# Kernel tuning notes

Measured on AMD Instinct MI355X. Metric: run time of the kernel, lower is better.

The kernel has to match this reference:

```python
import jax, jax.numpy as jnp
import numpy as np

B, L, C = 4, 6400, 768
HS, WS = 80, 80
NH, NP, NL = 6, 4, 1
DH = C // NH
EPS = 1e-6


def setup_inputs() -> dict:
    key = jax.random.key(0)
    ks = jax.random.split(key, 10)
    p = lambda k, shape: jax.random.normal(k, shape, jnp.float32) * 0.02
    return {
        "x": jax.random.normal(ks[0], (B, L, C), jnp.float32),
        "reference_points": jax.random.uniform(ks[1], (B, L, NL, 2), dtype=jnp.float32),
        "feat": jax.random.normal(ks[2], (B, L, C), jnp.float32),
        "spatial_shapes": jnp.array([[HS, WS]], jnp.int32),
        "level_start_index": jnp.array([0], jnp.int32),
        "qn_w": jnp.ones((C,), jnp.float32), "qn_b": jnp.zeros((C,), jnp.float32),
        "fn_w": jnp.ones((C,), jnp.float32), "fn_b": jnp.zeros((C,), jnp.float32),
        "gamma": p(ks[3], (C,)),
        "Wv": p(ks[4], (C, C)), "bv": jnp.zeros((C,), jnp.float32),
        "Woff": p(ks[5], (C, NH * NL * NP * 2)), "boff": p(ks[6], (NH * NL * NP * 2,)),
        "Waw": p(ks[7], (C, NH * NL * NP)), "baw": jnp.zeros((NH * NL * NP,), jnp.float32),
        "Wout": p(ks[8], (C, C)), "bout": jnp.zeros((C,), jnp.float32),
    }


def layernorm(x, w, b):
    mu = jnp.mean(x, -1, keepdims=True)
    var = jnp.mean((x - mu) ** 2, -1, keepdims=True)
    return (x - mu) * jax.lax.rsqrt(var + EPS) * w + b


def ms_deform_attn(q, reference_points, f, spatial_shapes, level_start_index,
                   Wv, bv, Woff, boff, Waw, baw, Wout, bout):
    shapes = np.asarray(spatial_shapes)      # static metadata (concrete)
    starts = np.asarray(level_start_index)
    value = (f @ Wv + bv).reshape(B, L, NH, DH)
    offs = (q @ Woff + boff).reshape(B, L, NH, NL, NP, 2)
    aw = jax.nn.softmax((q @ Waw + baw).reshape(B, L, NH, NL * NP), axis=-1)
    aw = aw.reshape(B, L, NH, NL, NP)
    # offset normalizer is (W, H) per level
    normalizer = jnp.stack([spatial_shapes[:, 1], spatial_shapes[:, 0]], -1).astype(q.dtype)
    loc = reference_points[:, :, None, :, None, :] + offs / normalizer[None, None, None, :, None, :]

    gat = jax.vmap(jax.vmap(lambda vv, ii: vv[ii]))  # over batch, then head
    levels = []
    for l in range(shapes.shape[0]):
        H_, W_ = int(shapes[l, 0]), int(shapes[l, 1])
        s0 = int(starts[l])
        v = value[:, s0:s0 + H_ * W_].transpose(0, 2, 1, 3)  # [B,NH,HW,DH]
        # grid_sample align_corners=False pixel coords
        lx = loc[:, :, :, l, :, 0] * W_ - 0.5                # [B,L,NH,NP]
        ly = loc[:, :, :, l, :, 1] * H_ - 0.5
        x0 = jnp.floor(lx); y0 = jnp.floor(ly)
        tx, ty = lx - x0, ly - y0
        x0i, y0i = x0.astype(jnp.int32), y0.astype(jnp.int32)
        acc = jnp.zeros((B, NH, L, NP, DH), value.dtype)
        for dy, wy in ((0, 1.0 - ty), (1, ty)):
            for dx, wx in ((0, 1.0 - tx), (1, tx)):
                xi, yi = x0i + dx, y0i + dy
                valid = (xi >= 0) & (xi < W_) & (yi >= 0) & (yi < H_)  # zero padding
                idx = (jnp.clip(yi, 0, H_ - 1) * W_ + jnp.clip(xi, 0, W_ - 1)).transpose(0, 2, 1, 3)
                w = (wx * wy * valid).transpose(0, 2, 1, 3)           # [B,NH,L,NP]
                acc = acc + gat(v, idx) * w[..., None]
        levels.append(acc)                                            # [B,NH,L,NP,DH]
    samp = jnp.stack(levels, axis=3)                                  # [B,NH,L,NL,NP,DH]
    out = jnp.einsum('bhqlpd,bqhlp->bqhd', samp, aw).reshape(B, L, C)
    return out @ Wout + bout


def reference(x, reference_points, feat, spatial_shapes, level_start_index,
              qn_w, qn_b, fn_w, fn_b, gamma, Wv, bv, Woff, boff, Waw, baw, Wout, bout):
    q = layernorm(x, qn_w, qn_b)
    f = layernorm(feat, fn_w, fn_b)
    attn = ms_deform_attn(q, reference_points, f, spatial_shapes, level_start_index,
                          Wv, bv, Woff, boff, Waw, baw, Wout, bout)
    return x + gamma * attn
```

## Files before the change

kernel.cpp:

```cpp
#include <hip/hip_runtime.h>
#include <hip/hip_bf16.h>

#define B_  4
#define L_  6400
#define C_  768
#define NH_ 6
#define NP_ 4
#define DH_ 128
#define HW_ 80
#define M_  (B_*L_)

using f32x4  = float __attribute__((ext_vector_type(4)));
using bf16x8 = short __attribute__((ext_vector_type(8)));

#define AS1(p) ((const __attribute__((address_space(1))) void*)(p))
#define AS3(p) ((__attribute__((address_space(3))) void*)(p))

__device__ __forceinline__ ushort f2bf(float f) {
    __hip_bfloat16 h = __float2bfloat16(f);
    return *reinterpret_cast<ushort*>(&h);
}
__device__ __forceinline__ float bf2f(ushort u) {
    union { unsigned u; float f; } v; v.u = ((unsigned)u) << 16; return v.f;
}

__global__ __launch_bounds__(256) void prep_weights(
    const float* __restrict__ Wv, const float* __restrict__ Woff,
    const float* __restrict__ Waw, const float* __restrict__ boff,
    const float* __restrict__ baw, const float* __restrict__ Wout,
    ushort* __restrict__ Wv_t, ushort* __restrict__ Wout_t,
    ushort* __restrict__ Wcomb_t, float* __restrict__ comb_bias)
{
    int i = blockIdx.x * 256 + threadIdx.x;
    const int WSZ = C_ * C_;
    if (i < WSZ) {
        int n = i / C_, k = i % C_;
        Wv_t[i]   = f2bf(Wv[k * C_ + n]);
        Wout_t[i] = f2bf(Wout[k * C_ + n]);
    } else {
        int j = i - WSZ;
        if (j < 128 * C_) {
            int n = j / C_, k = j % C_;
            float v = 0.f;
            if (n < 48)      v = Woff[k * 48 + n];
            else if (n < 72) v = Waw[k * 24 + (n - 48)];
            Wcomb_t[j] = f2bf(v);
        }
    }
    if (i < 128) {
        float v = 0.f;
        if (i < 48)      v = boff[i];
        else if (i < 72) v = baw[i - 48];
        comb_bias[i] = v;
    }
}

__global__ __launch_bounds__(256) void ln_kernel(
    const float* __restrict__ x, const float* __restrict__ feat,
    const float* __restrict__ qw, const float* __restrict__ qb,
    const float* __restrict__ fw, const float* __restrict__ fb,
    ushort* __restrict__ q, ushort* __restrict__ fn)
{
    int wave = threadIdx.x >> 6, lane = threadIdx.x & 63;
    long r = (long)blockIdx.x * 4 + wave;
    const float* in; ushort* out; const float* w; const float* b;
    if (r < M_) { in = x + r * C_;          out = q  + r * C_;          w = qw; b = qb; }
    else        { long rr = r - M_; in = feat + rr * C_; out = fn + rr * C_; w = fw; b = fb; }

    const float4* in4 = (const float4*)in;
    float4 v[3];
    float s = 0.f, s2 = 0.f;
#pragma unroll
    for (int i = 0; i < 3; i++) {
        v[i] = in4[lane + 64 * i];
        s  += v[i].x + v[i].y + v[i].z + v[i].w;
        s2 += v[i].x*v[i].x + v[i].y*v[i].y + v[i].z*v[i].z + v[i].w*v[i].w;
    }
#pragma unroll
    for (int off = 32; off; off >>= 1) { s += __shfl_xor(s, off); s2 += __shfl_xor(s2, off); }
    float mean = s * (1.f / C_);
    float var  = s2 * (1.f / C_) - mean * mean;
    float rs   = rsqrtf(var + 1e-6f);
#pragma unroll
    for (int i = 0; i < 3; i++) {
        int c = (lane + 64 * i) * 4;
        ushort4 o;
        o.x = f2bf((v[i].x - mean) * rs * w[c + 0] + b[c + 0]);
        o.y = f2bf((v[i].y - mean) * rs * w[c + 1] + b[c + 1]);
        o.z = f2bf((v[i].z - mean) * rs * w[c + 2] + b[c + 2]);
        o.w = f2bf((v[i].w - mean) * rs * w[c + 3] + b[c + 3]);
        ((ushort4*)out)[lane + 64 * i] = o;
    }
}

template<int MODE>
__global__ __launch_bounds__(256) void gemm_bf16(
    const ushort* __restrict__ A, const ushort* __restrict__ Bt,
    const float* __restrict__ bias, void* __restrict__ Cout,
    const float* __restrict__ xres, const float* __restrict__ gamma,
    int ldc)
{
    const int K = C_;
    __shared__ ushort As[128][32];
    __shared__ ushort Bs[128][32];
    const int m0 = blockIdx.y * 128;
    const int n0 = blockIdx.x * 128;
    const int t   = threadIdx.x;
    const int w   = t >> 6, lane = t & 63;
    const int WR = (w >> 1) * 64, WC = (w & 1) * 64;
    const int rowA0 = t >> 2;
    const int colA  = (t & 3) * 8;
    const int row15 = lane & 15, kb = (lane >> 4) * 8;

    f32x4 acc[4][4] = {};
    char* ldsA = (char*)As;
    char* ldsB = (char*)Bs;

    for (int k0 = 0; k0 < K; k0 += 32) {
        __syncthreads();
#pragma unroll
        for (int c = 0; c < 2; c++) {
            const ushort* ga = A  + (long)(m0 + c * 64 + rowA0) * K + k0 + colA;
            const ushort* gb = Bt + (long)(n0 + c * 64 + rowA0) * K + k0 + colA;
            __builtin_amdgcn_global_load_lds(AS1(ga), AS3(ldsA + c * 4096 + w * 1024), 16, 0, 0);
            __builtin_amdgcn_global_load_lds(AS1(gb), AS3(ldsB + c * 4096 + w * 1024), 16, 0, 0);
        }
        __syncthreads();
        bf16x8 af[4], bfr[4];
#pragma unroll
        for (int m = 0; m < 4; m++) af[m]  = *(bf16x8*)&As[WR + m * 16 + row15][kb];
#pragma unroll
        for (int n = 0; n < 4; n++) bfr[n] = *(bf16x8*)&Bs[WC + n * 16 + row15][kb];
#pragma unroll
        for (int m = 0; m < 4; m++)
#pragma unroll
            for (int n = 0; n < 4; n++)
                acc[m][n] = __builtin_amdgcn_mfma_f32_16x16x32_bf16(af[m], bfr[n], acc[m][n], 0, 0, 0);
    }

    const int rbase = (lane >> 4) * 4;
    const int cbase = lane & 15;
    const int bblk = m0 / L_;
#pragma unroll
    for (int m = 0; m < 4; m++)
#pragma unroll
    for (int n = 0; n < 4; n++) {
        int gcol = n0 + WC + n * 16 + cbase;
        float bb = bias[gcol];
#pragma unroll
        for (int j = 0; j < 4; j++) {
            int grow = m0 + WR + m * 16 + rbase + j;
            float vv = acc[m][n][j] + bb;
            if (MODE == 0) {
                int l = grow - bblk * L_;
                int h = gcol >> 7, d = gcol & 127;
                long o = (((long)bblk * NH_ + h) * L_ + l) * DH_ + d;
                ((ushort*)Cout)[o] = f2bf(vv);
            } else if (MODE == 1) {
                ((float*)Cout)[(long)grow * ldc + gcol] = vv;
            } else {
                long o = (long)grow * C_ + gcol;
                ((float*)Cout)[o] = xres[o] + gamma[gcol] * vv;
            }
        }
    }
}

__global__ __launch_bounds__(256) void loc_kernel(
    const float* __restrict__ scores,
    const float* __restrict__ refp,
    float4* __restrict__ samp)
{
    int wave = threadIdx.x >> 6, lane = threadIdx.x & 63;
    long row = (long)blockIdx.x * 4 + wave;
    if (lane >= 24) return;
    const float* sc = scores + row * 128;
    int h = lane >> 2, p = lane & 3;
    float ox = sc[h * 8 + p * 2], oy = sc[h * 8 + p * 2 + 1];
    float logit = sc[48 + lane];
    float m = logit;
    m = fmaxf(m, __shfl_xor(m, 1));
    m = fmaxf(m, __shfl_xor(m, 2));
    float e = expf(logit - m);
    float ssum = e;
    ssum += __shfl_xor(ssum, 1);
    ssum += __shfl_xor(ssum, 2);
    float w = e / ssum;
    float rx = refp[row * 2], ry = refp[row * 2 + 1];
    samp[row * 24 + lane] = make_float4(rx * HW_ + ox - 0.5f, ry * HW_ + oy - 0.5f, w, 0.f);
}

__global__ __launch_bounds__(256) void sample_kernel(
    const ushort* __restrict__ value_t,
    const float4* __restrict__ samp,
    ushort* __restrict__ attn_out)
{
    int wave = threadIdx.x >> 6, lane = threadIdx.x & 63;
    int gid = blockIdx.x * 4 + wave;
    int bh = gid / L_;  int l = gid - bh * L_;
    int b  = bh / NH_;  int h = bh - b * NH_;
    const ushort* plane = value_t + (long)bh * (HW_ * HW_) * DH_;
    long bl = (long)b * L_ + l;
    const float4* sp = samp + bl * 24 + h * 4;
    float acc0 = 0.f, acc1 = 0.f;
#pragma unroll
    for (int p = 0; p < 4; p++) {
        float4 s = sp[p];
        float lx = s.x, ly = s.y, wgt = s.z;
        float x0f = floorf(lx), y0f = floorf(ly);
        float tx = lx - x0f, ty = ly - y0f;
        int x0 = (int)x0f, y0 = (int)y0f;
#pragma unroll
        for (int dy = 0; dy < 2; dy++) {
            int yi = y0 + dy;
            if (yi < 0 || yi >= HW_) continue;
            float wy = dy ? ty : 1.f - ty;
#pragma unroll
            for (int dx = 0; dx < 2; dx++) {
                int xi = x0 + dx;
                if (xi < 0 || xi >= HW_) continue;
                float wx = dx ? tx : 1.f - tx;
                float wcr = wgt * wy * wx;
                int idx = __builtin_amdgcn_readfirstlane(yi * HW_ + xi);
                unsigned v = *(const unsigned*)(plane + (long)idx * DH_ + lane * 2);
                acc0 += wcr * bf2f((ushort)(v & 0xffffu));
                acc1 += wcr * bf2f((ushort)(v >> 16));
            }
        }
    }
    unsigned o = ((unsigned)f2bf(acc1) << 16) | (unsigned)f2bf(acc0);
    *(unsigned*)(attn_out + bl * C_ + h * DH_ + lane * 2) = o;
}

extern "C" void kernel_launch(void* const* d_in, const int* in_sizes, int n_in,
                              void* d_out, int out_size, void* d_ws, size_t ws_size,
                              hipStream_t stream) {
    const float* x     = (const float*)d_in[0];
    const float* refp  = (const float*)d_in[1];
    const float* feat  = (const float*)d_in[2];
    const float* qn_w  = (const float*)d_in[5];
    const float* qn_b  = (const float*)d_in[6];
    const float* fn_w  = (const float*)d_in[7];
    const float* fn_b  = (const float*)d_in[8];
    const float* gamma = (const float*)d_in[9];
    const float* Wv    = (const float*)d_in[10];
    const float* bv    = (const float*)d_in[11];
    const float* Woff  = (const float*)d_in[12];
    const float* boff  = (const float*)d_in[13];
    const float* Waw   = (const float*)d_in[14];
    const float* baw   = (const float*)d_in[15];
    const float* Wout  = (const float*)d_in[16];
    const float* bout  = (const float*)d_in[17];

    char* ws = (char*)d_ws;
    size_t off = 0;
    auto alloc = [&](size_t bytes) -> void* {
        void* p = ws + off; off += (bytes + 255) & ~(size_t)255; return p;
    };
    ushort* q       = (ushort*)alloc((size_t)M_ * C_ * 2);
    ushort* fn      = (ushort*)alloc((size_t)M_ * C_ * 2);
    ushort* value_t = (ushort*)alloc((size_t)M_ * C_ * 2);
    float4* samp    = (float4*)alloc((size_t)M_ * 24 * 16);
    ushort* Wv_t    = (ushort*)alloc((size_t)C_ * C_ * 2);
    ushort* Wout_t  = (ushort*)alloc((size_t)C_ * C_ * 2);
    ushort* Wcomb_t = (ushort*)alloc((size_t)128 * C_ * 2);
    float*  cbias   = (float*)alloc(128 * 4);
    float*  scores   = (float*)fn;
    ushort* attn_out = q;

    prep_weights<<<2688, 256, 0, stream>>>(Wv, Woff, Waw, boff, baw, Wout,
                                           Wv_t, Wout_t, Wcomb_t, cbias);
    ln_kernel<<<(2 * M_) / 4, 256, 0, stream>>>(x, feat, qn_w, qn_b, fn_w, fn_b, q, fn);
    gemm_bf16<0><<<dim3(6, 200), 256, 0, stream>>>(fn, Wv_t, bv, value_t, nullptr, nullptr, C_);
    gemm_bf16<1><<<dim3(1, 200), 256, 0, stream>>>(q, Wcomb_t, cbias, scores, nullptr, nullptr, 128);
    loc_kernel<<<M_ / 4, 256, 0, stream>>>(scores, refp, samp);
    sample_kernel<<<(M_ * NH_) / 4, 256, 0, stream>>>(value_t, samp, attn_out);
    gemm_bf16<2><<<dim3(6, 200), 256, 0, stream>>>(attn_out, Wout_t, bout, d_out, x, gamma, C_);
}
```

Measured before the change: 524.3 us.

## Use 16 threads per sample with 128-bit loads and XCD-aware block remap

Restructures the deformable sampling kernel so each query-head is handled by 16 threads loading 8 bf16 channels (uint4) each, instead of a full wave loading 2 channels each. Out-of-bounds taps are now clamped with a zero weight rather than branched around, so every tap is loaded without divergence. Block IDs are remapped so that contiguous work lands on the same XCD, aiming for better L2 locality of the value planes. The trade-off is more registers per thread and loads of clamped taps that contribute nothing.

```diff
diff --git a/kernel.cpp b/kernel.cpp
--- a/kernel.cpp
+++ b/kernel.cpp
@@ -195,14 +195,18 @@
     const float4* __restrict__ samp,
     ushort* __restrict__ attn_out)
 {
-    int wave = threadIdx.x >> 6, lane = threadIdx.x & 63;
-    int gid = blockIdx.x * 4 + wave;
+    int bid = (int)(blockIdx.x & 7) * 1200 + (int)(blockIdx.x >> 3);
+    int t = threadIdx.x;
+    int grp = t >> 4;
+    int d16 = t & 15;
+    int gid = bid * 16 + grp;
     int bh = gid / L_;  int l = gid - bh * L_;
     int b  = bh / NH_;  int h = bh - b * NH_;
-    const ushort* plane = value_t + (long)bh * (HW_ * HW_) * DH_;
+    const ushort* plane = value_t + (long)bh * (HW_ * HW_) * DH_ + d16 * 8;
     long bl = (long)b * L_ + l;
     const float4* sp = samp + bl * 24 + h * 4;
-    float acc0 = 0.f, acc1 = 0.f;
+
+    float acc[8] = {};
 #pragma unroll
     for (int p = 0; p < 4; p++) {
         float4 s = sp[p];
@@ -213,23 +217,32 @@
 #pragma unroll
         for (int dy = 0; dy < 2; dy++) {
             int yi = y0 + dy;
-            if (yi < 0 || yi >= HW_) continue;
             float wy = dy ? ty : 1.f - ty;
 #pragma unroll
             for (int dx = 0; dx < 2; dx++) {
                 int xi = x0 + dx;
-                if (xi < 0 || xi >= HW_) continue;
                 float wx = dx ? tx : 1.f - tx;
-                float wcr = wgt * wy * wx;
-                int idx = __builtin_amdgcn_readfirstlane(yi * HW_ + xi);
-                unsigned v = *(const unsigned*)(plane + (long)idx * DH_ + lane * 2);
-                acc0 += wcr * bf2f((ushort)(v & 0xffffu));
-                acc1 += wcr * bf2f((ushort)(v >> 16));
+                bool valid = (xi >= 0) & (xi < HW_) & (yi >= 0) & (yi < HW_);
+                float wc = valid ? (wgt * wy * wx) : 0.f;
+                int yc = min(max(yi, 0), HW_ - 1);
+                int xc = min(max(xi, 0), HW_ - 1);
+                uint4 v = *(const uint4*)(plane + (long)(yc * HW_ + xc) * DH_);
+                const unsigned* u = (const unsigned*)&v;
+#pragma unroll
+                for (int i = 0; i < 4; i++) {
+                    union { unsigned q; float f; } lo, hi;
+                    lo.q = u[i] << 16;
+                    hi.q = u[i] & 0xffff0000u;
+                    acc[2 * i]     += wc * lo.f;
+                    acc[2 * i + 1] += wc * hi.f;
+                }
             }
         }
     }
-    unsigned o = ((unsigned)f2bf(acc1) << 16) | (unsigned)f2bf(acc0);
-    *(unsigned*)(attn_out + bl * C_ + h * DH_ + lane * 2) = o;
+    bf16x8 o;
+#pragma unroll
+    for (int i = 0; i < 8; i++) o[i] = (short)f2bf(acc[i]);
+    *(bf16x8*)(attn_out + bl * C_ + h * DH_ + d16 * 8) = o;
 }
 
 extern "C" void kernel_launch(void* const* d_in, const int* in_sizes, int n_in,
@@ -274,6 +287,6 @@
     gemm_bf16<0><<<dim3(6, 200), 256, 0, stream>>>(fn, Wv_t, bv, value_t, nullptr, nullptr, C_);
     gemm_bf16<1><<<dim3(1, 200), 256, 0, stream>>>(q, Wcomb_t, cbias, scores, nullptr, nullptr, 128);
     loc_kernel<<<M_ / 4, 256, 0, stream>>>(scores, refp, samp);
-    sample_kernel<<<(M_ * NH_) / 4, 256, 0, stream>>>(value_t, samp, attn_out);
+    sample_kernel<<<(M_ * NH_) / 16, 256, 0, stream>>>(value_t, samp, attn_out);
     gemm_bf16<2><<<dim3(6, 200), 256, 0, stream>>>(attn_out, Wout_t, bout, d_out, x, gamma, C_);
 }
```

New measurement: 433.4 us. 17.3% less time.
